# Optimization experiments

Hardware: AMD Instinct MI355X
Metric: run time of the kernel (lower is better)

Reference implementation:

```python
import jax, jax.numpy as jnp
import numpy as np

D_MODEL = 1024
N_HEADS = 16
D_HEAD = D_MODEL // N_HEADS


def setup_inputs() -> dict:
    key = jax.random.key(0)
    k1, k2, k3 = jax.random.split(key, 3)
    B, T = 4, 2048
    x = jax.random.normal(k1, (B, T, D_MODEL), dtype=jnp.float32)
    # torch nn.Linear weights: (out_features, in_features), scaled init
    w_qkv = jax.random.normal(k2, (3 * D_MODEL, D_MODEL), dtype=jnp.float32) / np.sqrt(D_MODEL)
    w_out = jax.random.normal(k3, (D_MODEL, D_MODEL), dtype=jnp.float32) / np.sqrt(D_MODEL)
    return {"x": x, "w_qkv": w_qkv, "w_out": w_out}


def reference(x, w_qkv, w_out):
    B, T, _ = x.shape
    qkv = jnp.einsum('btd,ed->bte', x, w_qkv)  # (B,T,3*d_model)
    q, k, v = jnp.split(qkv, 3, axis=-1)
    # (B,T,H,dh) -> (B,H,T,dh)
    def heads(t):
        return t.reshape(B, T, N_HEADS, D_HEAD).transpose(0, 2, 1, 3)
    q, k, v = heads(q), heads(k), heads(v)
    scores = jnp.einsum('bhqd,bhkd->bhqk', q, k) / jnp.sqrt(jnp.float32(D_HEAD))
    causal = jnp.tril(jnp.ones((T, T), dtype=bool))  # True = keep
    scores = jnp.where(causal, scores, -jnp.inf)
    weights = jax.nn.softmax(scores, axis=-1)
    out = jnp.einsum('bhqk,bhkd->bhqd', weights, v)
    out = out.transpose(0, 2, 1, 3).reshape(B, T, D_MODEL)
    return jnp.einsum('btd,ed->bte', out, w_out)
```

## Files before the change

### kernel.cpp

```cpp
#include <hip/hip_runtime.h>

typedef __attribute__((ext_vector_type(8))) short short8;
typedef __attribute__((ext_vector_type(4))) float f32x4;
typedef __attribute__((ext_vector_type(4))) unsigned short us4;
typedef unsigned short u16;

#define MFMA16(a, b, c) __builtin_amdgcn_mfma_f32_16x16x32_bf16(a, b, c, 0, 0, 0)

static __device__ __forceinline__ u16 f2bf(float f) {
  union { float f; unsigned u; } v; v.f = f;
  unsigned r = v.u + 0x7fffu + ((v.u >> 16) & 1u);
  return (u16)(r >> 16);
}

static __device__ __forceinline__ unsigned cvtpk(float lo, float hi) {
  unsigned r;
  asm("v_cvt_pk_bf16_f32 %0, %1, %2" : "=v"(r) : "v"(lo), "v"(hi));
  return r;
}

static __device__ __forceinline__ void gl_lds16(const u16* g, u16* l) {
  __builtin_amdgcn_global_load_lds((const __attribute__((address_space(1))) void*)g,
                                   (__attribute__((address_space(3))) void*)l,
                                   16, 0, 0);
}

__global__ __launch_bounds__(256)
void cvt_bf16(const float* __restrict__ src, u16* __restrict__ dst, int n8)
{
  int i = blockIdx.x * 256 + threadIdx.x;
  const int stride = gridDim.x * 256;
  for (; i < n8; i += stride) {
    f32x4 a = ((const f32x4*)src)[2 * i];
    f32x4 b = ((const f32x4*)src)[2 * i + 1];
    short8 o;
    o[0] = (short)f2bf(a[0]); o[1] = (short)f2bf(a[1]);
    o[2] = (short)f2bf(a[2]); o[3] = (short)f2bf(a[3]);
    o[4] = (short)f2bf(b[0]); o[5] = (short)f2bf(b[1]);
    o[6] = (short)f2bf(b[2]); o[7] = (short)f2bf(b[3]);
    ((short8*)dst)[i] = o;
  }
}

__global__ __launch_bounds__(512, 2)
void gemm256_qkv(const u16* __restrict__ A, const u16* __restrict__ B,
                 u16* __restrict__ outp)
{
  __shared__ u16 Ash[2][8192];
  __shared__ u16 Bsh[2][8192];

  const int tid = threadIdx.x;
  const int lane = tid & 63;
  const int l15 = lane & 15, g = lane >> 4;
  const int w = tid >> 6;
  const int wr = w >> 2, wc = w & 3;

  const int bid = blockIdx.x;
  const int xcd = bid & 7, idx = bid >> 3;
  const int cx = xcd & 3, cy = xcd >> 2;
  const int mt = cx * 8 + (idx & 7);
  const int nt = cy * 6 + (idx >> 3);
  const long m0 = (long)mt * 256;
  const long n0 = (long)nt * 256;

  f32x4 acc[8][4] = {};

  const int c0 = tid, c1 = tid + 512;
  const int li0 = c0 >> 3, lp0 = (c0 & 7) ^ (li0 & 7);
  const int li1 = c1 >> 3, lp1 = (c1 & 7) ^ (li1 & 7);
  const int r0 = 2 * li0 + (lp0 >> 2), e0 = (lp0 & 3) * 8;
  const int r1 = 2 * li1 + (lp1 >> 2), e1 = (lp1 & 3) * 8;
  const u16* pa0 = A + (m0 + r0) * 1024 + e0;
  const u16* pa1 = A + (m0 + r1) * 1024 + e1;
  const u16* pb0 = B + (n0 + r0) * 1024 + e0;
  const u16* pb1 = B + (n0 + r1) * 1024 + e1;

  int aoff[8], boff[4];
  #pragma unroll
  for (int mi = 0; mi < 8; ++mi) {
    int row = wr * 128 + mi * 16 + l15;
    int line = row >> 1;
    int p = (((row & 1) << 2) | g) ^ (line & 7);
    aoff[mi] = line * 64 + p * 8;
  }
  #pragma unroll
  for (int nj = 0; nj < 4; ++nj) {
    int row = wc * 64 + nj * 16 + l15;
    int line = row >> 1;
    int p = (((row & 1) << 2) | g) ^ (line & 7);
    boff[nj] = line * 64 + p * 8;
  }

#define STAGE(kt, b) do {                              \
    gl_lds16(pa0 + (kt) * 32, &Ash[b][c0 * 8]);        \
    gl_lds16(pa1 + (kt) * 32, &Ash[b][c1 * 8]);        \
    gl_lds16(pb0 + (kt) * 32, &Bsh[b][c0 * 8]);        \
    gl_lds16(pb1 + (kt) * 32, &Bsh[b][c1 * 8]);        \
  } while (0)

  STAGE(0, 0);
  STAGE(1, 1);
  int cur = 0;

  for (int kt = 0; kt < 32; ++kt) {
    if (kt < 31) {
      asm volatile("s_waitcnt vmcnt(4)" ::: "memory");
    } else {
      asm volatile("s_waitcnt vmcnt(0)" ::: "memory");
    }
    __builtin_amdgcn_sched_barrier(0);
    __builtin_amdgcn_s_barrier();
    __builtin_amdgcn_sched_barrier(0);

    const u16* Ab = &Ash[cur][0];
    const u16* Bb = &Bsh[cur][0];
    short8 bf[4], af[8];
    #pragma unroll
    for (int nj = 0; nj < 4; ++nj) bf[nj] = *(const short8*)&Bb[boff[nj]];
    #pragma unroll
    for (int mi = 0; mi < 8; ++mi) af[mi] = *(const short8*)&Ab[aoff[mi]];
    __builtin_amdgcn_s_setprio(1);
    #pragma unroll
    for (int mi = 0; mi < 8; ++mi)
      #pragma unroll
      for (int nj = 0; nj < 4; ++nj)
        acc[mi][nj] = MFMA16(af[mi], bf[nj], acc[mi][nj]);
    __builtin_amdgcn_s_setprio(0);

    __builtin_amdgcn_sched_barrier(0);
    __builtin_amdgcn_s_barrier();
    __builtin_amdgcn_sched_barrier(0);
    if (kt < 30) STAGE(kt + 2, cur);
    cur ^= 1;
  }
#undef STAGE

  #pragma unroll
  for (int mi = 0; mi < 8; ++mi) {
    long m = m0 + wr * 128 + mi * 16 + g * 4;
    int b = (int)(m >> 11);
    int t = (int)(m & 2047);
    #pragma unroll
    for (int nj = 0; nj < 4; ++nj) {
      int e = (int)n0 + wc * 64 + nj * 16 + l15;
      int sel = e >> 10;
      int ee = e & 1023;
      int h = ee >> 6, dh = ee & 63;
      size_t bh131k = (size_t)(b * 16 + h) * 131072u;
      if (sel < 2) {
        float sc = (sel == 0) ? 0.125f : 1.0f;
        size_t base = (size_t)sel * 8388608u + bh131k + (size_t)t * 64u + dh;
        #pragma unroll
        for (int r = 0; r < 4; ++r)
          outp[base + (size_t)r * 64u] = f2bf(acc[mi][nj][r] * sc);
      } else {
        size_t base = 16777216u + bh131k + (size_t)dh * 2048u + (size_t)t;
        us4 v;
        #pragma unroll
        for (int r = 0; r < 4; ++r) v[r] = f2bf(acc[mi][nj][r]);
        *(us4*)&outp[base] = v;
      }
    }
  }
}

__global__ __launch_bounds__(256)
void gemm_out(const u16* __restrict__ A, const u16* __restrict__ B,
              float* __restrict__ outf)
{
  __shared__ u16 Ash[128 * 32];
  __shared__ u16 Bsh[128 * 32];
  const int tid = threadIdx.x;
  const int lane = tid & 63;
  const int l15 = lane & 15, g = lane >> 4;
  const int w = tid >> 6;
  const int wr = w >> 1, wc = w & 1;

  const int bid = blockIdx.x;
  const int xcd = bid & 7, idx = bid >> 3;
  const int cx = xcd & 3, cy = xcd >> 2;
  const int mt = cx * 16 + (idx & 15);
  const int nt = cy * 4 + (idx >> 4);
  const long m0 = (long)mt * 128;
  const long n0 = (long)nt * 128;

  f32x4 acc[4][4] = {};

  const int c0 = tid, c1 = tid + 256;
  const long arow0 = m0 + (c0 >> 2), arow1 = m0 + (c1 >> 2);
  int b0 = (int)(arow0 >> 11), t0 = (int)(arow0 & 2047);
  int b1 = (int)(arow1 >> 11), t1 = (int)(arow1 & 2047);
  const u16* pa0 = A + (size_t)(b0 * 16) * 131072u + (size_t)t0 * 64u + (c0 & 3) * 8;
  const u16* pa1 = A + (size_t)(b1 * 16) * 131072u + (size_t)t1 * 64u + (c1 & 3) * 8;
  const u16* pb0 = B + (n0 + (c0 >> 2)) * 1024 + (c0 & 3) * 8;
  const u16* pb1 = B + (n0 + (c1 >> 2)) * 1024 + (c1 & 3) * 8;
  u16* la0 = Ash + c0 * 8;
  u16* la1 = Ash + c1 * 8;
  u16* lb0 = Bsh + c0 * 8;
  u16* lb1 = Bsh + c1 * 8;

  const u16* afp[4];
  const u16* bfp[4];
  #pragma unroll
  for (int mi = 0; mi < 4; ++mi)
    afp[mi] = &Ash[(wr * 64 + mi * 16 + l15) * 32 + g * 8];
  #pragma unroll
  for (int ni = 0; ni < 4; ++ni)
    bfp[ni] = &Bsh[(wc * 64 + ni * 16 + l15) * 32 + g * 8];

  for (int k0 = 0; k0 < 1024; k0 += 32) {
    __syncthreads();
    gl_lds16(pa0, la0); gl_lds16(pa1, la1);
    gl_lds16(pb0, lb0); gl_lds16(pb1, lb1);
    long d = (k0 & 32) ? (131072 - 32) : 32;
    pa0 += d; pa1 += d;
    pb0 += 32; pb1 += 32;
    __syncthreads();

    short8 af[4], bf[4];
    #pragma unroll
    for (int mi = 0; mi < 4; ++mi) af[mi] = *(const short8*)afp[mi];
    #pragma unroll
    for (int ni = 0; ni < 4; ++ni) bf[ni] = *(const short8*)bfp[ni];
    #pragma unroll
    for (int mi = 0; mi < 4; ++mi)
      #pragma unroll
      for (int ni = 0; ni < 4; ++ni)
        acc[mi][ni] = MFMA16(af[mi], bf[ni], acc[mi][ni]);
  }

  #pragma unroll
  for (int mi = 0; mi < 4; ++mi) {
    long m = m0 + wr * 64 + mi * 16 + g * 4;
    #pragma unroll
    for (int ni = 0; ni < 4; ++ni) {
      int n = (int)n0 + wc * 64 + ni * 16 + l15;
      #pragma unroll
      for (int r = 0; r < 4; ++r)
        outf[(m + r) * 1024 + n] = acc[mi][ni][r];
    }
  }
}

__global__ __launch_bounds__(512, 4)
void attn(const u16* __restrict__ Q, const u16* __restrict__ K,
          const u16* __restrict__ VT, u16* __restrict__ O)
{
  __shared__ u16 Ksh[2][64 * 64];
  __shared__ u16 Vsh[2][64 * 64];
  __shared__ u16 Psh[8][16 * 64];

  const int tid = threadIdx.x;
  const int lane = tid & 63;
  const int l15 = lane & 15, g = lane >> 4;
  const int w = tid >> 6;
  const int bid = blockIdx.x;
  const int qi = 7 - (bid >> 6);
  const int bh = bid & 63;
  const int q0 = qi * 256;
  const int qb = q0 + w * 32;
  const int nt = qi * 4 + 4;

  const u16* Qp = Q + (size_t)bh * 131072u;
  const u16* Kp = K + (size_t)bh * 131072u;
  const u16* Vp = VT + (size_t)bh * 131072u;

  short8 qf[2][2];
  #pragma unroll
  for (int mi = 0; mi < 2; ++mi)
    #pragma unroll
    for (int kc = 0; kc < 2; ++kc)
      qf[mi][kc] = *(const short8*)&Qp[(qb + mi * 16 + l15) * 64 + kc * 32 + g * 8];

  f32x4 oacc[2][4] = {};
  float mrun[2] = {-1e30f, -1e30f};
  float lrun[2] = {0.f, 0.f};

  const int rA = tid >> 3, uA = ((tid & 7) ^ (rA & 7)) * 8;

#define STAGE(kv0s, b) do {                                            \
    gl_lds16(Kp + ((kv0s) + rA) * 64 + uA, Ksh[b] + tid * 8);          \
    gl_lds16(Vp + (size_t)rA * 2048u + (kv0s) + uA, Vsh[b] + tid * 8); \
  } while (0)

  STAGE(0, 0);
  int cur = 0;

  for (int ti = 0; ti < nt; ++ti) {
    const int kv0 = ti * 64;
    if (ti + 1 < nt) {
      STAGE(kv0 + 64, cur ^ 1);
      asm volatile("s_waitcnt vmcnt(2)" ::: "memory");
    } else {
      asm volatile("s_waitcnt vmcnt(0)" ::: "memory");
    }
    __builtin_amdgcn_s_barrier();
    __builtin_amdgcn_sched_barrier(0);

    if (kv0 <= qb + 31) {
      const u16* Kb = Ksh[cur];
      const u16* Vb = Vsh[cur];

      f32x4 s[2][4] = {};
      #pragma unroll
      for (int kc = 0; kc < 2; ++kc)
        #pragma unroll
        for (int ni = 0; ni < 4; ++ni) {
          int row = ni * 16 + l15;
          short8 kb = *(const short8*)&Kb[row * 64 + (((kc * 4 + g) ^ (row & 7)) << 3)];
          #pragma unroll
          for (int mi = 0; mi < 2; ++mi)
            s[mi][ni] = MFMA16(kb, qf[mi][kc], s[mi][ni]);
        }

      if (kv0 + 63 > qb) {
        #pragma unroll
        for (int mi = 0; mi < 2; ++mi) {
          int qv = qb + mi * 16 + l15;
          #pragma unroll
          for (int ni = 0; ni < 4; ++ni)
            #pragma unroll
            for (int r = 0; r < 4; ++r)
              if (kv0 + ni * 16 + g * 4 + r > qv)
                s[mi][ni][r] = -1e30f;
        }
      }

      #pragma unroll
      for (int mi = 0; mi < 2; ++mi) {
        float mx0 = fmaxf(fmaxf(s[mi][0][0], s[mi][0][1]),
                          fmaxf(s[mi][0][2], s[mi][0][3]));
        float mx1 = fmaxf(fmaxf(s[mi][1][0], s[mi][1][1]),
                          fmaxf(s[mi][1][2], s[mi][1][3]));
        float mx2 = fmaxf(fmaxf(s[mi][2][0], s[mi][2][1]),
                          fmaxf(s[mi][2][2], s[mi][2][3]));
        float mx3 = fmaxf(fmaxf(s[mi][3][0], s[mi][3][1]),
                          fmaxf(s[mi][3][2], s[mi][3][3]));
        float mx = fmaxf(fmaxf(mx0, mx1), fmaxf(mx2, mx3));
        mx = fmaxf(mx, __shfl_xor(mx, 16));
        mx = fmaxf(mx, __shfl_xor(mx, 32));
        if (!__all(mx - mrun[mi] <= 8.0f)) {
          float mn = fmaxf(mrun[mi], mx);
          float sc = __expf(mrun[mi] - mn);
          mrun[mi] = mn;
          lrun[mi] *= sc;
          #pragma unroll
          for (int nj = 0; nj < 4; ++nj) {
            oacc[mi][nj][0] *= sc;
            oacc[mi][nj][1] *= sc;
            oacc[mi][nj][2] *= sc;
            oacc[mi][nj][3] *= sc;
          }
        }
        float mn = mrun[mi];
        float rs = 0.f;
        #pragma unroll
        for (int ni = 0; ni < 4; ++ni)
          #pragma unroll
          for (int r = 0; r < 4; ++r) {
            float p = __expf(s[mi][ni][r] - mn);
            s[mi][ni][r] = p;
            rs += p;
          }
        rs += __shfl_xor(rs, 16);
        rs += __shfl_xor(rs, 32);
        lrun[mi] += rs;
      }

      u16* Pw = &Psh[w][0];
      short8 pb[2][2];
      #pragma unroll
      for (int mi = 0; mi < 2; ++mi) {
        #pragma unroll
        for (int ni = 0; ni < 4; ++ni) {
          int col = ni * 16 + g * 4;
          uint2 pv;
          pv.x = cvtpk(s[mi][ni][0], s[mi][ni][1]);
          pv.y = cvtpk(s[mi][ni][2], s[mi][ni][3]);
          *(uint2*)&Pw[l15 * 64 + (col ^ ((l15 & 7) << 3))] = pv;
        }
        #pragma unroll
        for (int kc = 0; kc < 2; ++kc)
          pb[mi][kc] = *(const short8*)&Pw[l15 * 64 + (((kc * 4 + g) ^ (l15 & 7)) << 3)];
      }

      #pragma unroll
      for (int kc = 0; kc < 2; ++kc)
        #pragma unroll
        for (int nj = 0; nj < 4; ++nj) {
          int vrow = nj * 16 + l15;
          short8 vb = *(const short8*)&Vb[vrow * 64 + (((kc * 4 + g) ^ (vrow & 7)) << 3)];
          #pragma unroll
          for (int mi = 0; mi < 2; ++mi)
            oacc[mi][nj] = MFMA16(vb, pb[mi][kc], oacc[mi][nj]);
        }
    }

    __builtin_amdgcn_sched_barrier(0);
    __builtin_amdgcn_s_barrier();
    cur ^= 1;
  }
#undef STAGE

  #pragma unroll
  for (int mi = 0; mi < 2; ++mi) {
    float inv = 1.0f / lrun[mi];
    int t = qb + mi * 16 + l15;
    size_t base = (size_t)bh * 131072u + (size_t)t * 64u;
    #pragma unroll
    for (int nj = 0; nj < 4; ++nj) {
      uint2 o;
      o.x = cvtpk(oacc[mi][nj][0] * inv, oacc[mi][nj][1] * inv);
      o.y = cvtpk(oacc[mi][nj][2] * inv, oacc[mi][nj][3] * inv);
      *(uint2*)&O[base + nj * 16 + g * 4] = o;
    }
  }
}

extern "C" void kernel_launch(void* const* d_in, const int* in_sizes, int n_in,
                              void* d_out, int out_size, void* d_ws, size_t ws_size,
                              hipStream_t stream)
{
  (void)in_sizes; (void)n_in; (void)out_size; (void)ws_size;
  const float* x    = (const float*)d_in[0];
  const float* wqkv = (const float*)d_in[1];
  const float* wout = (const float*)d_in[2];
  u16* ws  = (u16*)d_ws;
  u16* Qw   = ws;
  u16* Kw   = ws + 8388608;
  u16* VTw  = ws + 16777216;
  u16* wqb  = ws + 25165824;
  u16* wob  = ws + 28311552;
  u16* xb   = (u16*)d_out;
  float* y  = (float*)d_out;

  hipLaunchKernelGGL(cvt_bf16, dim3(2048), dim3(256), 0, stream, x,    xb,  1048576);
  hipLaunchKernelGGL(cvt_bf16, dim3(1536), dim3(256), 0, stream, wqkv, wqb, 393216);
  hipLaunchKernelGGL(cvt_bf16, dim3(512),  dim3(256), 0, stream, wout, wob, 131072);
  hipLaunchKernelGGL(gemm256_qkv, dim3(384), dim3(512), 0, stream, xb, wqb, ws);
  hipLaunchKernelGGL(attn,        dim3(512), dim3(512), 0, stream, Qw, Kw, VTw, Qw);
  hipLaunchKernelGGL(gemm_out,    dim3(512), dim3(256), 0, stream, Qw, wob, y);
}
```

Measured before the change: 198.0 us.

## Restructure QKV GEMM into 8-phase pipeline with K=64 tiles and dynamic LDS

Replaces the 256x256 QKV GEMM main loop with a version that stages K=64 per iteration in two 32-wide halves, using 128KB of dynamic LDS. Each iteration is split into four barrier-separated phases that interleave global-to-LDS loads with MFMA sub-blocks, so loads overlap compute at a finer grain. The LDS swizzle layout is also changed. A simpler 128x128 fallback kernel runs if the large dynamic-LDS attribute cannot be set, and a hipFuncSetAttribute call is now made on every launch.

```diff
diff --git a/kernel.cpp b/kernel.cpp
--- a/kernel.cpp
+++ b/kernel.cpp
@@ -24,6 +24,12 @@
                                    (__attribute__((address_space(3))) void*)l,
                                    16, 0, 0);
 }
+
+#define BAR() do { __builtin_amdgcn_sched_barrier(0); \
+                   __builtin_amdgcn_s_barrier();      \
+                   __builtin_amdgcn_sched_barrier(0); } while (0)
+#define LGK() do { asm volatile("s_waitcnt lgkmcnt(0)" ::: "memory"); \
+                   __builtin_amdgcn_sched_barrier(0); } while (0)
 
 __global__ __launch_bounds__(256)
 void cvt_bf16(const float* __restrict__ src, u16* __restrict__ dst, int n8)
@@ -42,99 +48,10 @@
   }
 }
 
-__global__ __launch_bounds__(512, 2)
-void gemm256_qkv(const u16* __restrict__ A, const u16* __restrict__ B,
-                 u16* __restrict__ outp)
-{
-  __shared__ u16 Ash[2][8192];
-  __shared__ u16 Bsh[2][8192];
-
-  const int tid = threadIdx.x;
-  const int lane = tid & 63;
-  const int l15 = lane & 15, g = lane >> 4;
-  const int w = tid >> 6;
-  const int wr = w >> 2, wc = w & 3;
-
-  const int bid = blockIdx.x;
-  const int xcd = bid & 7, idx = bid >> 3;
-  const int cx = xcd & 3, cy = xcd >> 2;
-  const int mt = cx * 8 + (idx & 7);
-  const int nt = cy * 6 + (idx >> 3);
-  const long m0 = (long)mt * 256;
-  const long n0 = (long)nt * 256;
-
-  f32x4 acc[8][4] = {};
-
-  const int c0 = tid, c1 = tid + 512;
-  const int li0 = c0 >> 3, lp0 = (c0 & 7) ^ (li0 & 7);
-  const int li1 = c1 >> 3, lp1 = (c1 & 7) ^ (li1 & 7);
-  const int r0 = 2 * li0 + (lp0 >> 2), e0 = (lp0 & 3) * 8;
-  const int r1 = 2 * li1 + (lp1 >> 2), e1 = (lp1 & 3) * 8;
-  const u16* pa0 = A + (m0 + r0) * 1024 + e0;
-  const u16* pa1 = A + (m0 + r1) * 1024 + e1;
-  const u16* pb0 = B + (n0 + r0) * 1024 + e0;
-  const u16* pb1 = B + (n0 + r1) * 1024 + e1;
-
-  int aoff[8], boff[4];
-  #pragma unroll
-  for (int mi = 0; mi < 8; ++mi) {
-    int row = wr * 128 + mi * 16 + l15;
-    int line = row >> 1;
-    int p = (((row & 1) << 2) | g) ^ (line & 7);
-    aoff[mi] = line * 64 + p * 8;
-  }
-  #pragma unroll
-  for (int nj = 0; nj < 4; ++nj) {
-    int row = wc * 64 + nj * 16 + l15;
-    int line = row >> 1;
-    int p = (((row & 1) << 2) | g) ^ (line & 7);
-    boff[nj] = line * 64 + p * 8;
-  }
-
-#define STAGE(kt, b) do {                              \
-    gl_lds16(pa0 + (kt) * 32, &Ash[b][c0 * 8]);        \
-    gl_lds16(pa1 + (kt) * 32, &Ash[b][c1 * 8]);        \
-    gl_lds16(pb0 + (kt) * 32, &Bsh[b][c0 * 8]);        \
-    gl_lds16(pb1 + (kt) * 32, &Bsh[b][c1 * 8]);        \
-  } while (0)
-
-  STAGE(0, 0);
-  STAGE(1, 1);
-  int cur = 0;
-
-  for (int kt = 0; kt < 32; ++kt) {
-    if (kt < 31) {
-      asm volatile("s_waitcnt vmcnt(4)" ::: "memory");
-    } else {
-      asm volatile("s_waitcnt vmcnt(0)" ::: "memory");
-    }
-    __builtin_amdgcn_sched_barrier(0);
-    __builtin_amdgcn_s_barrier();
-    __builtin_amdgcn_sched_barrier(0);
-
-    const u16* Ab = &Ash[cur][0];
-    const u16* Bb = &Bsh[cur][0];
-    short8 bf[4], af[8];
-    #pragma unroll
-    for (int nj = 0; nj < 4; ++nj) bf[nj] = *(const short8*)&Bb[boff[nj]];
-    #pragma unroll
-    for (int mi = 0; mi < 8; ++mi) af[mi] = *(const short8*)&Ab[aoff[mi]];
-    __builtin_amdgcn_s_setprio(1);
-    #pragma unroll
-    for (int mi = 0; mi < 8; ++mi)
-      #pragma unroll
-      for (int nj = 0; nj < 4; ++nj)
-        acc[mi][nj] = MFMA16(af[mi], bf[nj], acc[mi][nj]);
-    __builtin_amdgcn_s_setprio(0);
-
-    __builtin_amdgcn_sched_barrier(0);
-    __builtin_amdgcn_s_barrier();
-    __builtin_amdgcn_sched_barrier(0);
-    if (kt < 30) STAGE(kt + 2, cur);
-    cur ^= 1;
-  }
-#undef STAGE
-
+static __device__ __forceinline__ void qkv_scatter(
+    f32x4 (*acc)[4], u16* __restrict__ outp,
+    long m0, long n0, int wr, int wc, int l15, int g)
+{
   #pragma unroll
   for (int mi = 0; mi < 8; ++mi) {
     long m = m0 + wr * 128 + mi * 16 + g * 4;
@@ -158,6 +75,221 @@
         us4 v;
         #pragma unroll
         for (int r = 0; r < 4; ++r) v[r] = f2bf(acc[mi][nj][r]);
+        *(us4*)&outp[base] = v;
+      }
+    }
+  }
+}
+
+__global__ __launch_bounds__(512, 2)
+void gemm8p_qkv(const u16* __restrict__ A, const u16* __restrict__ B,
+                u16* __restrict__ outp)
+{
+  extern __shared__ u16 lds[];
+
+  const int tid = threadIdx.x;
+  const int lane = tid & 63;
+  const int l15 = lane & 15, g = lane >> 4;
+  const int w = tid >> 6;
+  const int wr = w >> 2, wc = w & 3;
+
+  const int bid = blockIdx.x;
+  const int xcd = bid & 7, idx = bid >> 3;
+  const int cx = xcd & 3, cy = xcd >> 2;
+  const int mt = cx * 8 + (idx & 7);
+  const int nt = cy * 6 + (idx >> 3);
+  const long m0 = (long)mt * 256;
+  const long n0 = (long)nt * 256;
+
+  f32x4 acc[8][4] = {};
+
+  const int c0 = tid, c1 = tid + 512;
+  const int ar0 = c0 >> 2, ap0 = (c0 & 3) ^ ((ar0 >> 1) & 3);
+  const int ar1 = c1 >> 2, ap1 = (c1 & 3) ^ ((ar1 >> 1) & 3);
+  const u16* sA0 = A + (m0 + ar0) * 1024 + ap0 * 8;
+  const u16* sA1 = A + (m0 + ar1) * 1024 + ap1 * 8;
+  const u16* sB0 = B + (n0 + ar0) * 1024 + ap0 * 8;
+  const u16* sB1 = B + (n0 + ar1) * 1024 + ap1 * 8;
+
+  int aoff[8], boff[4];
+  #pragma unroll
+  for (int mi = 0; mi < 8; ++mi) {
+    int r = wr * 128 + mi * 16 + l15;
+    aoff[mi] = r * 32 + (g ^ ((r >> 1) & 3)) * 8;
+  }
+  #pragma unroll
+  for (int nj = 0; nj < 4; ++nj) {
+    int r = wc * 64 + nj * 16 + l15;
+    boff[nj] = 16384 + r * 32 + (g ^ ((r >> 1) & 3)) * 8;
+  }
+
+#define ST_A(kt, b, kh) do { \
+    gl_lds16(sA0 + (kt) * 64 + (kh) * 32, &lds[(b) * 32768 + (kh) * 8192 + c0 * 8]); \
+    gl_lds16(sA1 + (kt) * 64 + (kh) * 32, &lds[(b) * 32768 + (kh) * 8192 + c1 * 8]); \
+  } while (0)
+#define ST_B(kt, b, kh) do { \
+    gl_lds16(sB0 + (kt) * 64 + (kh) * 32, &lds[(b) * 32768 + 16384 + (kh) * 8192 + c0 * 8]); \
+    gl_lds16(sB1 + (kt) * 64 + (kh) * 32, &lds[(b) * 32768 + 16384 + (kh) * 8192 + c1 * 8]); \
+  } while (0)
+
+  ST_A(0, 0, 0); ST_B(0, 0, 0); ST_A(0, 0, 1); ST_B(0, 0, 1);
+
+  for (int kt = 0; kt < 16; ++kt) {
+    const int b = kt & 1, nb = b ^ 1;
+    const bool more = (kt < 15);
+    const u16* L = lds + b * 32768;
+    short8 bf[4], af[4];
+
+    if (more) { ST_A(kt + 1, nb, 0);
+                asm volatile("s_waitcnt vmcnt(6)" ::: "memory"); }
+    else      { asm volatile("s_waitcnt vmcnt(4)" ::: "memory"); }
+    BAR();
+    #pragma unroll
+    for (int nj = 0; nj < 4; ++nj) bf[nj] = *(const short8*)&L[boff[nj]];
+    #pragma unroll
+    for (int mi = 0; mi < 4; ++mi) af[mi] = *(const short8*)&L[aoff[mi]];
+    LGK();
+    __builtin_amdgcn_s_setprio(1);
+    #pragma unroll
+    for (int mi = 0; mi < 4; ++mi)
+      #pragma unroll
+      for (int nj = 0; nj < 4; ++nj)
+        acc[mi][nj] = MFMA16(af[mi], bf[nj], acc[mi][nj]);
+    __builtin_amdgcn_s_setprio(0);
+
+    if (more) ST_B(kt + 1, nb, 0);
+    BAR();
+    #pragma unroll
+    for (int mi = 0; mi < 4; ++mi) af[mi] = *(const short8*)&L[aoff[mi + 4]];
+    LGK();
+    __builtin_amdgcn_s_setprio(1);
+    #pragma unroll
+    for (int mi = 0; mi < 4; ++mi)
+      #pragma unroll
+      for (int nj = 0; nj < 4; ++nj)
+        acc[mi + 4][nj] = MFMA16(af[mi], bf[nj], acc[mi + 4][nj]);
+    __builtin_amdgcn_s_setprio(0);
+
+    if (more) { ST_A(kt + 1, nb, 1);
+                asm volatile("s_waitcnt vmcnt(6)" ::: "memory"); }
+    else      { asm volatile("s_waitcnt vmcnt(0)" ::: "memory"); }
+    BAR();
+    #pragma unroll
+    for (int nj = 0; nj < 4; ++nj) bf[nj] = *(const short8*)&L[boff[nj] + 8192];
+    #pragma unroll
+    for (int mi = 0; mi < 4; ++mi) af[mi] = *(const short8*)&L[aoff[mi] + 8192];
+    LGK();
+    __builtin_amdgcn_s_setprio(1);
+    #pragma unroll
+    for (int mi = 0; mi < 4; ++mi)
+      #pragma unroll
+      for (int nj = 0; nj < 4; ++nj)
+        acc[mi][nj] = MFMA16(af[mi], bf[nj], acc[mi][nj]);
+    __builtin_amdgcn_s_setprio(0);
+
+    if (more) ST_B(kt + 1, nb, 1);
+    BAR();
+    #pragma unroll
+    for (int mi = 0; mi < 4; ++mi) af[mi] = *(const short8*)&L[aoff[mi + 4] + 8192];
+    LGK();
+    __builtin_amdgcn_s_setprio(1);
+    #pragma unroll
+    for (int mi = 0; mi < 4; ++mi)
+      #pragma unroll
+      for (int nj = 0; nj < 4; ++nj)
+        acc[mi + 4][nj] = MFMA16(af[mi], bf[nj], acc[mi + 4][nj]);
+    __builtin_amdgcn_s_setprio(0);
+
+    BAR();
+  }
+#undef ST_A
+#undef ST_B
+
+  qkv_scatter(acc, outp, m0, n0, wr, wc, l15, g);
+}
+
+__global__ __launch_bounds__(256)
+void gemm_qkv_fb(const u16* __restrict__ A, const u16* __restrict__ B,
+                 u16* __restrict__ outp)
+{
+  __shared__ u16 Ash[128 * 32];
+  __shared__ u16 Bsh[128 * 32];
+  const int tid = threadIdx.x;
+  const int lane = tid & 63;
+  const int l15 = lane & 15, g = lane >> 4;
+  const int w = tid >> 6;
+  const int wr = w >> 1, wc = w & 1;
+
+  const int bid = blockIdx.x;
+  const int xcd = bid & 7, idx = bid >> 3;
+  const int cx = xcd & 3, cy = xcd >> 2;
+  const int mt = cx * 16 + (idx & 15);
+  const int nt = cy * 12 + (idx >> 4);
+  const long m0 = (long)mt * 128;
+  const long n0 = (long)nt * 128;
+
+  f32x4 acc[4][4] = {};
+
+  const int c0 = tid, c1 = tid + 256;
+  const u16* pa0 = A + (m0 + (c0 >> 2)) * 1024 + (c0 & 3) * 8;
+  const u16* pa1 = A + (m0 + (c1 >> 2)) * 1024 + (c1 & 3) * 8;
+  const u16* pb0 = B + (n0 + (c0 >> 2)) * 1024 + (c0 & 3) * 8;
+  const u16* pb1 = B + (n0 + (c1 >> 2)) * 1024 + (c1 & 3) * 8;
+  u16* la0 = Ash + c0 * 8;
+  u16* la1 = Ash + c1 * 8;
+  u16* lb0 = Bsh + c0 * 8;
+  u16* lb1 = Bsh + c1 * 8;
+
+  const u16* afp[4];
+  const u16* bfp[4];
+  #pragma unroll
+  for (int mi = 0; mi < 4; ++mi)
+    afp[mi] = &Ash[(wr * 64 + mi * 16 + l15) * 32 + g * 8];
+  #pragma unroll
+  for (int ni = 0; ni < 4; ++ni)
+    bfp[ni] = &Bsh[(wc * 64 + ni * 16 + l15) * 32 + g * 8];
+
+  for (int k0 = 0; k0 < 1024; k0 += 32) {
+    __syncthreads();
+    gl_lds16(pa0, la0); gl_lds16(pa1, la1);
+    gl_lds16(pb0, lb0); gl_lds16(pb1, lb1);
+    pa0 += 32; pa1 += 32; pb0 += 32; pb1 += 32;
+    __syncthreads();
+    short8 af[4], bf[4];
+    #pragma unroll
+    for (int mi = 0; mi < 4; ++mi) af[mi] = *(const short8*)afp[mi];
+    #pragma unroll
+    for (int ni = 0; ni < 4; ++ni) bf[ni] = *(const short8*)bfp[ni];
+    #pragma unroll
+    for (int mi = 0; mi < 4; ++mi)
+      #pragma unroll
+      for (int ni = 0; ni < 4; ++ni)
+        acc[mi][ni] = MFMA16(af[mi], bf[ni], acc[mi][ni]);
+  }
+
+  #pragma unroll
+  for (int mi = 0; mi < 4; ++mi) {
+    long m = m0 + wr * 64 + mi * 16 + g * 4;
+    int b = (int)(m >> 11);
+    int t = (int)(m & 2047);
+    #pragma unroll
+    for (int ni = 0; ni < 4; ++ni) {
+      int e = (int)n0 + wc * 64 + ni * 16 + l15;
+      int sel = e >> 10;
+      int ee = e & 1023;
+      int h = ee >> 6, dh = ee & 63;
+      size_t bh131k = (size_t)(b * 16 + h) * 131072u;
+      if (sel < 2) {
+        float sc = (sel == 0) ? 0.125f : 1.0f;
+        size_t base = (size_t)sel * 8388608u + bh131k + (size_t)t * 64u + dh;
+        #pragma unroll
+        for (int r = 0; r < 4; ++r)
+          outp[base + (size_t)r * 64u] = f2bf(acc[mi][ni][r] * sc);
+      } else {
+        size_t base = 16777216u + bh131k + (size_t)dh * 2048u + (size_t)t;
+        us4 v;
+        #pragma unroll
+        for (int r = 0; r < 4; ++r) v[r] = f2bf(acc[mi][ni][r]);
         *(us4*)&outp[base] = v;
       }
     }
@@ -437,7 +569,15 @@
   hipLaunchKernelGGL(cvt_bf16, dim3(2048), dim3(256), 0, stream, x,    xb,  1048576);
   hipLaunchKernelGGL(cvt_bf16, dim3(1536), dim3(256), 0, stream, wqkv, wqb, 393216);
   hipLaunchKernelGGL(cvt_bf16, dim3(512),  dim3(256), 0, stream, wout, wob, 131072);
-  hipLaunchKernelGGL(gemm256_qkv, dim3(384), dim3(512), 0, stream, xb, wqb, ws);
-  hipLaunchKernelGGL(attn,        dim3(512), dim3(512), 0, stream, Qw, Kw, VTw, Qw);
-  hipLaunchKernelGGL(gemm_out,    dim3(512), dim3(256), 0, stream, Qw, wob, y);
-}
+
+  hipError_t e = hipFuncSetAttribute((const void*)gemm8p_qkv,
+                   hipFuncAttributeMaxDynamicSharedMemorySize, 131072);
+  if (e == hipSuccess) {
+    hipLaunchKernelGGL(gemm8p_qkv, dim3(384), dim3(512), 131072, stream, xb, wqb, ws);
+  } else {
+    hipLaunchKernelGGL(gemm_qkv_fb, dim3(1536), dim3(256), 0, stream, xb, wqb, ws);
+  }
+
+  hipLaunchKernelGGL(attn,     dim3(512), dim3(512), 0, stream, Qw, Kw, VTw, Qw);
+  hipLaunchKernelGGL(gemm_out, dim3(512), dim3(256), 0, stream, Qw, wob, y);
+}
```

After: 183.7 us. 7.2% less time.
